# Optimization experiments

Hardware: AMD Instinct MI355X
Metric: run time of the kernel (lower is better)

The kernel has to match this reference:

```python
import jax, jax.numpy as jnp
import numpy as np

EPS = 1e-5  # torch InstanceNorm2d default eps


def _attend(x_q, x_kv, Wq, Wk, Wv, Wo):
    # x_q, x_kv: [B, N, C]
    B, N, _ = x_q.shape
    q = x_q @ Wq            # [B, N, CH]
    k = x_kv @ Wk           # [B, N, CH]
    v = x_kv @ Wv           # [B, N, CH]
    CH = q.shape[-1]
    # rearrange 'b n c -> n (b c)' : [N, B*CH]; the torch repeat across batch
    # is redundant (same K/V for every query sample), so we keep one copy.
    kcat = jnp.transpose(k, (1, 0, 2)).reshape(N, B * CH)
    vcat = jnp.transpose(v, (1, 0, 2)).reshape(N, B * CH)
    # scores[b, i, j] = sum_n q[b, n, i] * kcat[n, j]  -> [B, CH, B*CH]
    scores = jnp.einsum('bni,nj->bij', q, kcat)
    # InstanceNorm2d(1): per-sample normalization over the (CH, B*CH) plane
    mu = scores.mean(axis=(1, 2), keepdims=True)
    var = scores.var(axis=(1, 2), keepdims=True)  # biased var, matches torch
    scores = (scores - mu) * jax.lax.rsqrt(var + EPS)
    attn = jax.nn.softmax(scores, axis=-1)        # softmax over j (dim=3)
    # ctx[b, n, i] = sum_j attn[b, i, j] * vcat[n, j]  -> [B, N, CH]
    ctx = jnp.einsum('bij,nj->bni', attn, vcat)
    return ctx @ Wo  # [B, N, C]


def setup_inputs() -> dict:
    key = jax.random.key(0)
    k0, k1, k2, k3, k4 = jax.random.split(key, 5)
    C, H = 64, 8
    CH = C * H
    emb = jax.random.normal(k0, (16, 2048, C), dtype=jnp.float32)
    s = 0.02
    Wq = jax.random.normal(k1, (C, CH), dtype=jnp.float32) * s
    Wk = jax.random.normal(k2, (C, CH), dtype=jnp.float32) * s
    Wv = jax.random.normal(k3, (C, CH), dtype=jnp.float32) * s
    Wo = jax.random.normal(k4, (CH, C), dtype=jnp.float32) * s
    return {"emb": emb, "Wq": Wq, "Wk": Wk, "Wv": Wv, "Wo": Wo}


def reference(emb, Wq, Wk, Wv, Wo):
    emb_l, emb_u = jnp.split(emb, 2, axis=0)
    emb_u_sg = jax.lax.stop_gradient(emb_u)  # emb_u is detached in the torch code
    out_u2l = _attend(emb_u_sg, emb_l, Wq, Wk, Wv, Wo)
    out_l2u = _attend(emb_l, emb_u_sg, Wq, Wk, Wv, Wo)
    return jnp.concatenate([out_l2u, out_u2l], axis=0)
```

## Files before the change

### kernel.cpp

```cpp
#include <hip/hip_runtime.h>
#include <hip/hip_fp16.h>

#define EPS 1e-5f

typedef __attribute__((ext_vector_type(8))) _Float16 half8;
typedef __attribute__((ext_vector_type(4))) _Float16 half4;
typedef __attribute__((ext_vector_type(4))) float float4v;

__device__ __forceinline__ float rv_from(const float* sums2, int db)
{
    float s1 = 0.f, s2 = 0.f;
#pragma unroll
    for (int p = 0; p < 8; p++) {
        s1 += sums2[(db * 8 + p) * 2];
        s2 += sums2[(db * 8 + p) * 2 + 1];
    }
    const float inv = 1.f / 2097152.f;
    float mu = s1 * inv;
    float var = s2 * inv - mu * mu;
    return rsqrtf(var + EPS);
}

__global__ __launch_bounds__(256)
void convT_k(const float* __restrict__ emb, const float* __restrict__ Wq,
             const float* __restrict__ Wk, const float* __restrict__ Wv,
             const float* __restrict__ Wo, __half* __restrict__ emb16,
             __half* __restrict__ embT16, __half* __restrict__ WkT16,
             __half* __restrict__ Wo16, __half* __restrict__ Wv16,
             float* __restrict__ GWQpart, float* __restrict__ wsp,
             __half* __restrict__ WqT16h, __half* __restrict__ WqT16l)
{
    __shared__ __align__(16) char smem[18432];
    const int tid = threadIdx.x;
    const int bid = blockIdx.x;

    if (bid < 256) {
        __half (*T)[136] = (__half(*)[136])smem;
        const int bb = bid >> 4;
        const int t0 = (bid & 15) * 128;
        const float* src = emb + (long long)bb * 131072 + (long long)t0 * 64;
        __half* d16 = emb16 + (long long)bb * 131072 + (long long)t0 * 64;
#pragma unroll
        for (int it = 0; it < 8; it++) {
            int e = (tid + it * 256) * 4;
            int t = e >> 6, c = e & 63;
            float4 v = *(const float4*)(src + t * 64 + c);
            half4 h;
            h[0] = (_Float16)v.x; h[1] = (_Float16)v.y;
            h[2] = (_Float16)v.z; h[3] = (_Float16)v.w;
            *(half4*)(d16 + t * 64 + c) = h;
            T[c + 0][t] = (__half)h[0];
            T[c + 1][t] = (__half)h[1];
            T[c + 2][t] = (__half)h[2];
            T[c + 3][t] = (__half)h[3];
        }
        __syncthreads();
        __half* dT = embT16 + (long long)bb * 131072 + t0;
#pragma unroll
        for (int it = 0; it < 4; it++) {
            int e = (tid + it * 256) * 8;
            int c = e >> 7, tt = e & 127;
            *(half8*)(dT + (long long)c * 2048 + tt) = *(const half8*)&T[c][tt];
        }
    } else if (bid < 272) {
        float (*t)[65] = (float(*)[65])smem;
        const int which = (bid - 256) >> 3;
        const int c0 = ((bid - 256) & 7) * 64;
        const int c = tid & 63, r4 = tid >> 6;
        if (which == 0) {
#pragma unroll
            for (int rr = r4; rr < 64; rr += 4)
                t[rr][c] = Wk[rr * 512 + c0 + c];
            __syncthreads();
#pragma unroll
            for (int rr = r4; rr < 64; rr += 4)
                WkT16[(c0 + rr) * 64 + c] = __float2half(t[c][rr]);
        } else {
#pragma unroll
            for (int rr = r4; rr < 64; rr += 4)
                t[rr][c] = Wo[(c0 + rr) * 64 + c];
            __syncthreads();
#pragma unroll
            for (int rr = r4; rr < 64; rr += 4)
                Wo16[rr * 512 + c0 + c] = __float2half(t[c][rr]);
        }
    } else if (bid < 280) {
        const int base = (bid - 272) * 4096;
#pragma unroll
        for (int it = 0; it < 4; it++) {
            int e = base + (tid + it * 256) * 4;
            float4 v = *(const float4*)(Wv + e);
            *(__half2*)(Wv16 + e)     = __floats2half2_rn(v.x, v.y);
            *(__half2*)(Wv16 + e + 2) = __floats2half2_rn(v.z, v.w);
        }
    } else if (bid < 296) {
        float (*Wl)[68] = (float(*)[68])smem;
        const int t2 = bid - 280;
        const int which = t2 >> 3;
        const int sl = t2 & 7;
        const int i0 = sl * 64;
        const float* W = which ? Wq : Wk;
        float* Gout = GWQpart + (long long)(which * 8 + sl) * 4096;
#pragma unroll
        for (int it = 0; it < 4; it++) {
            int e = tid + it * 256;
            int cc = e >> 4, i4 = (e & 15) * 4;
            *(float4*)&Wl[cc][i4] = *(const float4*)(W + cc * 512 + i0 + i4);
        }
        __syncthreads();
        if (tid < 64) {
            float s = 0.f;
#pragma unroll
            for (int j = 0; j < 64; j++) s += Wl[tid][j];
            wsp[(which * 8 + sl) * 64 + tid] = s;
        }
        const int cr = tid >> 2, cg = (tid & 3) * 16;
        float p[16] = {};
        for (int k = 0; k < 64; k++) {
            float a = Wl[cr][k];
#pragma unroll
            for (int j = 0; j < 16; j++) p[j] += a * Wl[cg + j][k];
        }
#pragma unroll
        for (int j = 0; j < 16; j++)
            Gout[cr * 64 + cg + j] = p[j];
    } else {
        float (*t)[65] = (float(*)[65])smem;
        const int i0 = (bid - 296) * 64;
        const int c = tid & 63, r4 = tid >> 6;
#pragma unroll
        for (int rr = r4; rr < 64; rr += 4)
            t[rr][c] = Wq[rr * 512 + i0 + c];
        __syncthreads();
#pragma unroll
        for (int rr = r4; rr < 64; rr += 4) {
            float x = t[c][rr];
            __half h = __float2half(x);
            WqT16h[(i0 + rr) * 64 + c] = h;
            WqT16l[(i0 + rr) * 64 + c] = __float2half(x - __half2float(h));
        }
    }
}

__global__ __launch_bounds__(256)
void gram_k(const __half* __restrict__ embT16, float* __restrict__ Gpart)
{
    const int tid = threadIdx.x, bid = blockIdx.x;
    const int ks = bid >> 6, z6 = bid & 63;
    const int b = z6 >> 3, bp = z6 & 7;
    const int lane = tid & 63, w = tid >> 6, q = lane >> 4, l16 = lane & 15;

    const __half* Arow = embT16 + (long long)b * 131072 +
                         (long long)(w * 16 + l16) * 2048 + ks * 256 + q * 8;
    const __half* Bbase = embT16 + 1048576 + (long long)bp * 131072 +
                          (long long)l16 * 2048 + ks * 256 + q * 8;

    float4v acc[4];
#pragma unroll
    for (int nt = 0; nt < 4; nt++) acc[nt] = (float4v)0.f;

#pragma unroll
    for (int t0 = 0; t0 < 256; t0 += 32) {
        half8 af = *(const half8*)(Arow + t0);
        half8 bf[4];
#pragma unroll
        for (int nt = 0; nt < 4; nt++)
            bf[nt] = *(const half8*)(Bbase + nt * 32768 + t0);
#pragma unroll
        for (int nt = 0; nt < 4; nt++)
            acc[nt] = __builtin_amdgcn_mfma_f32_16x16x32_f16(af, bf[nt], acc[nt], 0, 0, 0);
    }

    float* Gz = Gpart + (long long)ks * 262144 + (long long)z6 * 4096;
#pragma unroll
    for (int nt = 0; nt < 4; nt++)
#pragma unroll
        for (int t = 0; t < 4; t++) {
            int m = w * 16 + q * 4 + t;
            Gz[m * 64 + nt * 16 + l16] = acc[nt][t];
        }
}

__global__ __launch_bounds__(256)
void stats2_k(const float* __restrict__ Gpart, const float* __restrict__ GWQpart,
              const float* __restrict__ wsp, __half* __restrict__ GT16h,
              __half* __restrict__ GT16l, float* __restrict__ sums2)
{
    __shared__ float Graw[64][68], Gs[64][68], GQs[64][68], GWs[64][68];
    __shared__ float wqsS[64], wksS[64];
    const int tid = threadIdx.x;
    const int z = blockIdx.x;
    const int d = z >> 6, b = (z >> 3) & 7, bp = z & 7;
    const int zm = d ? (bp * 8 + b) : (b * 8 + bp);

    for (int f = tid * 4; f < 4096; f += 1024) {
        float4 g = make_float4(0.f, 0.f, 0.f, 0.f);
        float4 gw = g, gq = g;
#pragma unroll
        for (int s = 0; s < 8; s++) {
            float4 p = *(const float4*)(Gpart + (long long)s * 262144 + (long long)zm * 4096 + f);
            g.x += p.x; g.y += p.y; g.z += p.z; g.w += p.w;
            float4 w1 = *(const float4*)(GWQpart + (long long)s * 4096 + f);
            gw.x += w1.x; gw.y += w1.y; gw.z += w1.z; gw.w += w1.w;
            float4 q1 = *(const float4*)(GWQpart + (long long)(8 + s) * 4096 + f);
            gq.x += q1.x; gq.y += q1.y; gq.z += q1.z; gq.w += q1.w;
        }
        int rr = f >> 6, cc = f & 63;
        *(float4*)&Graw[rr][cc] = g;
        *(float4*)&GWs[rr][cc] = gw;
        *(float4*)&GQs[rr][cc] = gq;
    }
    if (tid < 64) {
        float a = 0.f, bsum = 0.f;
#pragma unroll
        for (int s = 0; s < 8; s++) {
            bsum += wsp[s * 64 + tid];
            a    += wsp[(8 + s) * 64 + tid];
        }
        wqsS[tid] = a; wksS[tid] = bsum;
    }
    __syncthreads();
    for (int e = tid; e < 4096; e += 256) {
        int rr = e >> 6, cc = e & 63;
        Gs[rr][cc] = d ? Graw[cc][rr] : Graw[rr][cc];
    }
    __syncthreads();
    for (int e = tid; e < 4096; e += 256) {
        int cp = e >> 6, c = e & 63;
        float g = Gs[c][cp];
        __half h = __float2half(g);
        GT16h[(long long)z * 4096 + e] = h;
        GT16l[(long long)z * 4096 + e] = __float2half(g - __half2float(h));
    }

    const int r = tid >> 2;
    const int c0 = (tid & 3) * 16;
    float p1[16] = {}, p2[16] = {};
    for (int k = 0; k < 64; k++) {
        float gq = GQs[r][k], g = Gs[r][k];
#pragma unroll
        for (int j = 0; j < 16; j++) {
            p1[j] += gq * Gs[k][c0 + j];
            p2[j] += g  * GWs[k][c0 + j];
        }
    }
    float s2 = 0.f;
#pragma unroll
    for (int j = 0; j < 16; j++) s2 += p1[j] * p2[j];
    float s1 = 0.f;
    const float wq = wqsS[r];
#pragma unroll
    for (int j = 0; j < 16; j++) s1 += wq * Gs[r][c0 + j] * wksS[c0 + j];

    const int lane = tid & 63, w = tid >> 6;
#pragma unroll
    for (int off = 32; off; off >>= 1) {
        s1 += __shfl_down(s1, off, 64);
        s2 += __shfl_down(s2, off, 64);
    }
    __shared__ float r1[4], r2[4];
    if (lane == 0) { r1[w] = s1; r2[w] = s2; }
    __syncthreads();
    if (tid == 0) {
        sums2[z * 2]     = r1[0] + r1[1] + r1[2] + r1[3];
        sums2[z * 2 + 1] = r2[0] + r2[1] + r2[2] + r2[3];
    }
}

__global__ __launch_bounds__(256)
void mfma_ms(const __half* __restrict__ WqT16h, const __half* __restrict__ WqT16l,
             const __half* __restrict__ GT16h, const __half* __restrict__ GT16l,
             const __half* __restrict__ WkT16, const __half* __restrict__ Wv16,
             const float* __restrict__ sums2, float* __restrict__ rsp,
             __half* __restrict__ Mt)
{
    __shared__ __half Es[128][72];
    __shared__ __half Pt[128][72];

    const int tid = threadIdx.x;
    const int z = blockIdx.x;
    const int it = blockIdx.y;
    const int db = z >> 3, bp = z & 7;
    const int i0base = it * 128;

    const int lane = tid & 63, w = tid >> 6, q = lane >> 4, l16 = lane & 15;
    const float rv = rv_from(sums2, db);

    {
        const __half* Wh = WqT16h + (long long)i0base * 64;
        const __half* Wl = WqT16l + (long long)i0base * 64;
        const __half* Gh = GT16h + (long long)z * 4096;
        const __half* Gl = GT16l + (long long)z * 4096;
        float4v eacc[2][4];
#pragma unroll
        for (int a = 0; a < 2; a++)
#pragma unroll
            for (int b2 = 0; b2 < 4; b2++) eacc[a][b2] = (float4v)0.f;
#pragma unroll
        for (int kc = 0; kc < 64; kc += 32) {
            half8 ah[2], al[2], bh[4], bl[4];
#pragma unroll
            for (int mt = 0; mt < 2; mt++) {
                const int i = w * 32 + mt * 16 + l16;
                ah[mt] = *(const half8*)(Wh + i * 64 + kc + q * 8);
                al[mt] = *(const half8*)(Wl + i * 64 + kc + q * 8);
            }
#pragma unroll
            for (int nt = 0; nt < 4; nt++) {
                const int cp = nt * 16 + l16;
                bh[nt] = *(const half8*)(Gh + cp * 64 + kc + q * 8);
                bl[nt] = *(const half8*)(Gl + cp * 64 + kc + q * 8);
            }
#pragma unroll
            for (int mt = 0; mt < 2; mt++)
#pragma unroll
                for (int nt = 0; nt < 4; nt++) {
                    eacc[mt][nt] = __builtin_amdgcn_mfma_f32_16x16x32_f16(ah[mt], bh[nt], eacc[mt][nt], 0, 0, 0);
                    eacc[mt][nt] = __builtin_amdgcn_mfma_f32_16x16x32_f16(ah[mt], bl[nt], eacc[mt][nt], 0, 0, 0);
                    eacc[mt][nt] = __builtin_amdgcn_mfma_f32_16x16x32_f16(al[mt], bh[nt], eacc[mt][nt], 0, 0, 0);
                }
        }
#pragma unroll
        for (int mt = 0; mt < 2; mt++)
#pragma unroll
            for (int nt = 0; nt < 4; nt++)
#pragma unroll
                for (int t = 0; t < 4; t++)
                    Es[w * 32 + mt * 16 + q * 4 + t][nt * 16 + l16] =
                        __float2half(eacc[mt][nt][t]);
    }

    float4v macc[2][4];
#pragma unroll
    for (int a = 0; a < 2; a++)
#pragma unroll
        for (int b2 = 0; b2 < 4; b2++) macc[a][b2] = (float4v)0.f;
    float rsacc[2] = {0.f, 0.f};

    for (int ch0 = 0; ch0 < 512; ch0 += 64) {
        float4v sacc[4][2];
#pragma unroll
        for (int a = 0; a < 4; a++)
#pragma unroll
            for (int b2 = 0; b2 < 2; b2++) sacc[a][b2] = (float4v)0.f;
#pragma unroll
        for (int kc = 0; kc < 64; kc += 32) {
            half8 af[4], bf[2];
#pragma unroll
            for (int mt = 0; mt < 4; mt++)
                af[mt] = *(const half8*)(WkT16 +
                    (long long)(ch0 + mt * 16 + l16) * 64 + kc + q * 8);
#pragma unroll
            for (int nt = 0; nt < 2; nt++)
                bf[nt] = *(const half8*)&Es[w * 32 + nt * 16 + l16][kc + q * 8];
#pragma unroll
            for (int mt = 0; mt < 4; mt++)
#pragma unroll
                for (int nt = 0; nt < 2; nt++)
                    sacc[mt][nt] = __builtin_amdgcn_mfma_f32_16x16x32_f16(af[mt], bf[nt], sacc[mt][nt], 0, 0, 0);
        }

#pragma unroll
        for (int nt = 0; nt < 2; nt++) {
            const int i = w * 32 + nt * 16 + l16;
#pragma unroll
            for (int mt = 0; mt < 4; mt++) {
                float e0 = __expf(rv * sacc[mt][nt][0]);
                float e1 = __expf(rv * sacc[mt][nt][1]);
                float e2 = __expf(rv * sacc[mt][nt][2]);
                float e3 = __expf(rv * sacc[mt][nt][3]);
                rsacc[nt] += e0 + e1 + e2 + e3;
                const int ch = mt * 16 + q * 4;
                *(__half2*)&Pt[i][ch]     = __floats2half2_rn(e0, e1);
                *(__half2*)&Pt[i][ch + 2] = __floats2half2_rn(e2, e3);
            }
        }

#pragma unroll
        for (int kc = 0; kc < 64; kc += 32) {
            half8 af2[2], bf2[4];
#pragma unroll
            for (int mt2 = 0; mt2 < 2; mt2++)
                af2[mt2] = *(const half8*)&Pt[w * 32 + mt2 * 16 + l16][kc + q * 8];
#pragma unroll
            for (int nt2 = 0; nt2 < 4; nt2++)
                bf2[nt2] = *(const half8*)(Wv16 +
                    (long long)(nt2 * 16 + l16) * 512 + ch0 + kc + q * 8);
#pragma unroll
            for (int mt2 = 0; mt2 < 2; mt2++)
#pragma unroll
                for (int nt2 = 0; nt2 < 4; nt2++)
                    macc[mt2][nt2] = __builtin_amdgcn_mfma_f32_16x16x32_f16(af2[mt2], bf2[nt2], macc[mt2][nt2], 0, 0, 0);
        }
    }

#pragma unroll
    for (int nt = 0; nt < 2; nt++) {
        float p = rsacc[nt];
        p += __shfl_xor(p, 16, 64);
        p += __shfl_xor(p, 32, 64);
        if (q == 0)
            rsp[(long long)(db * 512 + i0base + w * 32 + nt * 16 + l16) * 8 + bp] = p;
    }
    __syncthreads();

    __half (*MtS)[144] = (__half(*)[144])&Pt[0][0];
    const float sc = 1.f / 4096.f;
#pragma unroll
    for (int mt2 = 0; mt2 < 2; mt2++)
#pragma unroll
        for (int nt2 = 0; nt2 < 4; nt2++) {
            const int cp = nt2 * 16 + l16;
            const int il = w * 32 + mt2 * 16 + q * 4;
#pragma unroll
            for (int t = 0; t < 4; t++)
                MtS[cp][il + t] = __float2half(macc[mt2][nt2][t] * sc);
        }
    __syncthreads();
    __half* Mz = Mt + (long long)z * 32768;
    {
        const int row = tid >> 2, seg = (tid & 3) * 32;
#pragma unroll
        for (int j = 0; j < 4; j++)
            *(half8*)(Mz + (long long)row * 512 + i0base + seg + j * 8) =
                *(const half8*)&MtS[row][seg + j * 8];
    }
}

__global__ __launch_bounds__(256)
void mfma_n(const __half* __restrict__ Mt, const __half* __restrict__ Wo16,
            const float* __restrict__ rsp, __half* __restrict__ NT)
{
    __shared__ __half Mts[64][72];
    __shared__ __half Wos[64][72];
    __shared__ float invrS[64];
    const int tid = threadIdx.x;
    const int db = blockIdx.x >> 3, bp = blockIdx.x & 7;
    const __half* Mz = Mt + (long long)(db * 8 + bp) * 32768;
    const int lane = tid & 63, w = tid >> 6, q = lane >> 4, l16 = lane & 15;

    float4v acc[4];
#pragma unroll
    for (int mt = 0; mt < 4; mt++) acc[mt] = (float4v)0.f;

    const int srow = tid >> 2, sc8 = (tid & 3) * 16;

    for (int i0 = 0; i0 < 512; i0 += 64) {
        __syncthreads();
        if (tid < 64) {
            const float* rp = rsp + (long long)(db * 512 + i0 + tid) * 8;
            float4 a = *(const float4*)rp;
            float4 b = *(const float4*)(rp + 4);
            invrS[tid] = 4096.0f / (a.x + a.y + a.z + a.w + b.x + b.y + b.z + b.w);
        }
        __syncthreads();
#pragma unroll
        for (int h = 0; h < 2; h++) {
            half8 v = *(const half8*)(Mz + (long long)srow * 512 + i0 + sc8 + h * 8);
            half8 o;
#pragma unroll
            for (int j = 0; j < 8; j++)
                o[j] = (_Float16)((float)v[j] * invrS[sc8 + h * 8 + j]);
            *(half8*)&Mts[srow][sc8 + h * 8] = o;
            *(half8*)&Wos[srow][sc8 + h * 8] =
                *(const half8*)(Wo16 + (long long)srow * 512 + i0 + sc8 + h * 8);
        }
        __syncthreads();
#pragma unroll
        for (int kc = 0; kc < 64; kc += 32) {
            half8 af[4];
#pragma unroll
            for (int mt = 0; mt < 4; mt++)
                af[mt] = *(const half8*)&Mts[mt * 16 + l16][kc + q * 8];
            half8 bf = *(const half8*)&Wos[w * 16 + l16][kc + q * 8];
#pragma unroll
            for (int mt = 0; mt < 4; mt++)
                acc[mt] = __builtin_amdgcn_mfma_f32_16x16x32_f16(af[mt], bf, acc[mt], 0, 0, 0);
        }
    }

    __half* Nz = NT + (long long)db * 32768;
    const int o = w * 16 + l16;
#pragma unroll
    for (int mt = 0; mt < 4; mt++) {
        const int k = bp * 64 + mt * 16 + q * 4;
        *(__half2*)(Nz + (long long)o * 512 + k)     = __floats2half2_rn(acc[mt][0], acc[mt][1]);
        *(__half2*)(Nz + (long long)o * 512 + k + 2) = __floats2half2_rn(acc[mt][2], acc[mt][3]);
    }
}

__global__ __launch_bounds__(256)
void mfma_out(const __half* __restrict__ emb16, const __half* __restrict__ NT,
              float* __restrict__ out)
{
    const int tid = threadIdx.x;
    const int db = blockIdx.y;
    const int d = db >> 3;
    const int n0 = blockIdx.x * 128;
    const __half* Xb = emb16 + (long long)(1 - d) * 1048576;
    const __half* Bz = NT + (long long)db * 32768;

    const int lane = tid & 63, w = tid >> 6, q = lane >> 4, l16 = lane & 15;

    float4v acc[2][4];
#pragma unroll
    for (int a = 0; a < 2; a++)
#pragma unroll
        for (int b = 0; b < 4; b++) acc[a][b] = (float4v)0.f;

    for (int bp = 0; bp < 8; bp++) {
        const __half* src = Xb + (long long)bp * 131072 + (long long)n0 * 64;
#pragma unroll
        for (int kc = 0; kc < 64; kc += 32) {
            half8 af[2], bf[4];
#pragma unroll
            for (int mt = 0; mt < 2; mt++)
                af[mt] = *(const half8*)(src + (long long)(w * 32 + mt * 16 + l16) * 64 + kc + q * 8);
#pragma unroll
            for (int ot = 0; ot < 4; ot++)
                bf[ot] = *(const half8*)(Bz + (long long)(ot * 16 + l16) * 512 + bp * 64 + kc + q * 8);
#pragma unroll
            for (int mt = 0; mt < 2; mt++)
#pragma unroll
                for (int ot = 0; ot < 4; ot++)
                    acc[mt][ot] = __builtin_amdgcn_mfma_f32_16x16x32_f16(af[mt], bf[ot], acc[mt][ot], 0, 0, 0);
        }
    }

    float* Od = out + (long long)db * 131072;
#pragma unroll
    for (int mt = 0; mt < 2; mt++)
#pragma unroll
        for (int ot = 0; ot < 4; ot++)
#pragma unroll
            for (int t = 0; t < 4; t++) {
                int n = n0 + w * 32 + mt * 16 + q * 4 + t;
                Od[(long long)n * 64 + ot * 16 + l16] = acc[mt][ot][t];
            }
}

extern "C" void kernel_launch(void* const* d_in, const int* in_sizes, int n_in,
                              void* d_out, int out_size, void* d_ws, size_t ws_size,
                              hipStream_t stream)
{
    const float* emb = (const float*)d_in[0];
    const float* Wq  = (const float*)d_in[1];
    const float* Wk  = (const float*)d_in[2];
    const float* Wv  = (const float*)d_in[3];
    const float* Wo  = (const float*)d_in[4];
    float* out = (float*)d_out;
    float* ws  = (float*)d_ws;

    float* Gpart   = ws;
    float* GWQpart = ws + 2097152;
    float* wsp     = ws + 2162688;
    float* sums2   = ws + 2163712;
    __half* GT16h  = (__half*)(ws + 2163968);
    __half* GT16l  = (__half*)(ws + 2426112);
    float* rsp     = ws + 2688256;
    __half* WkT16  = (__half*)(ws + 2753792);
    __half* Wv16   = (__half*)(ws + 2770176);
    __half* Wo16   = (__half*)(ws + 2786560);
    __half* WqT16h = (__half*)(ws + 2802944);
    __half* WqT16l = (__half*)(ws + 2819328);
    __half* Mt     = (__half*)(ws + 2835712);
    __half* NT     = (__half*)(ws + 4932864);
    __half* emb16  = (__half*)(ws + 5195008);
    __half* embT16 = (__half*)(ws + 6243584);

    convT_k<<<304, 256, 0, stream>>>(emb, Wq, Wk, Wv, Wo, emb16, embT16,
                                     WkT16, Wo16, Wv16, GWQpart, wsp,
                                     WqT16h, WqT16l);

    gram_k<<<512, 256, 0, stream>>>(embT16, Gpart);

    stats2_k<<<128, 256, 0, stream>>>(Gpart, GWQpart, wsp, GT16h, GT16l, sums2);

    mfma_ms<<<dim3(128, 4), 256, 0, stream>>>(WqT16h, WqT16l, GT16h, GT16l,
                                              WkT16, Wv16, sums2, rsp, Mt);

    mfma_n<<<128, 256, 0, stream>>>(Mt, Wo16, rsp, NT);

    mfma_out<<<dim3(16, 16), 256, 0, stream>>>(emb16, NT, out);
}
```

Measured before the change: 171.0 us.

## Double-buffer Wk and Wv tiles in LDS with register prefetch in mfma_ms

Each 64-channel chunk of WkT16 and Wv16 is now staged into double-buffered shared memory, with the next chunk prefetched into registers while the current chunk is computed. This replaces redundant per-wave global loads of the weight fragments with one cooperative load per block, and hides global latency. The cost is about 36KB of extra LDS, which may reduce occupancy, and a block-wide barrier on every iteration.

```diff
diff --git a/kernel.cpp b/kernel.cpp
--- a/kernel.cpp
+++ b/kernel.cpp
@@ -275,6 +275,8 @@
              __half* __restrict__ Mt)
 {
     __shared__ __half Es[128][72];
+    __shared__ __half Wks[2][64][72];
+    __shared__ __half Wvs[2][64][72];
     __shared__ __half Pt[128][72];
 
     const int tid = threadIdx.x;
@@ -285,6 +287,12 @@
 
     const int lane = tid & 63, w = tid >> 6, q = lane >> 4, l16 = lane & 15;
     const float rv = rv_from(sums2, db);
+    const int srow = tid >> 2, sc8 = (tid & 3) * 16;
+
+    half8 gk0 = *(const half8*)(WkT16 + (long long)srow * 64 + sc8);
+    half8 gk1 = *(const half8*)(WkT16 + (long long)srow * 64 + sc8 + 8);
+    half8 gv0 = *(const half8*)(Wv16 + (long long)srow * 512 + sc8);
+    half8 gv1 = *(const half8*)(Wv16 + (long long)srow * 512 + sc8 + 8);
 
     {
         const __half* Wh = WqT16h + (long long)i0base * 64;
@@ -329,6 +337,11 @@
                     Es[w * 32 + mt * 16 + q * 4 + t][nt * 16 + l16] =
                         __float2half(eacc[mt][nt][t]);
     }
+    *(half8*)&Wks[0][srow][sc8]     = gk0;
+    *(half8*)&Wks[0][srow][sc8 + 8] = gk1;
+    *(half8*)&Wvs[0][srow][sc8]     = gv0;
+    *(half8*)&Wvs[0][srow][sc8 + 8] = gv1;
+    __syncthreads();
 
     float4v macc[2][4];
 #pragma unroll
@@ -337,7 +350,17 @@
         for (int b2 = 0; b2 < 4; b2++) macc[a][b2] = (float4v)0.f;
     float rsacc[2] = {0.f, 0.f};
 
-    for (int ch0 = 0; ch0 < 512; ch0 += 64) {
+    int cur = 0;
+    for (int c = 0; c < 8; c++) {
+        const int ch0 = c * 64;
+        if (c < 7) {
+            const int chn = ch0 + 64;
+            gk0 = *(const half8*)(WkT16 + (long long)(chn + srow) * 64 + sc8);
+            gk1 = *(const half8*)(WkT16 + (long long)(chn + srow) * 64 + sc8 + 8);
+            gv0 = *(const half8*)(Wv16 + (long long)srow * 512 + chn + sc8);
+            gv1 = *(const half8*)(Wv16 + (long long)srow * 512 + chn + sc8 + 8);
+        }
+
         float4v sacc[4][2];
 #pragma unroll
         for (int a = 0; a < 4; a++)
@@ -348,8 +371,7 @@
             half8 af[4], bf[2];
 #pragma unroll
             for (int mt = 0; mt < 4; mt++)
-                af[mt] = *(const half8*)(WkT16 +
-                    (long long)(ch0 + mt * 16 + l16) * 64 + kc + q * 8);
+                af[mt] = *(const half8*)&Wks[cur][mt * 16 + l16][kc + q * 8];
 #pragma unroll
             for (int nt = 0; nt < 2; nt++)
                 bf[nt] = *(const half8*)&Es[w * 32 + nt * 16 + l16][kc + q * 8];
@@ -384,14 +406,22 @@
                 af2[mt2] = *(const half8*)&Pt[w * 32 + mt2 * 16 + l16][kc + q * 8];
 #pragma unroll
             for (int nt2 = 0; nt2 < 4; nt2++)
-                bf2[nt2] = *(const half8*)(Wv16 +
-                    (long long)(nt2 * 16 + l16) * 512 + ch0 + kc + q * 8);
+                bf2[nt2] = *(const half8*)&Wvs[cur][nt2 * 16 + l16][kc + q * 8];
 #pragma unroll
             for (int mt2 = 0; mt2 < 2; mt2++)
 #pragma unroll
                 for (int nt2 = 0; nt2 < 4; nt2++)
                     macc[mt2][nt2] = __builtin_amdgcn_mfma_f32_16x16x32_f16(af2[mt2], bf2[nt2], macc[mt2][nt2], 0, 0, 0);
         }
+
+        if (c < 7) {
+            *(half8*)&Wks[cur ^ 1][srow][sc8]     = gk0;
+            *(half8*)&Wks[cur ^ 1][srow][sc8 + 8] = gk1;
+            *(half8*)&Wvs[cur ^ 1][srow][sc8]     = gv0;
+            *(half8*)&Wvs[cur ^ 1][srow][sc8 + 8] = gv1;
+        }
+        __syncthreads();
+        cur ^= 1;
     }
 
 #pragma unroll
@@ -402,7 +432,6 @@
         if (q == 0)
             rsp[(long long)(db * 512 + i0base + w * 32 + nt * 16 + l16) * 8 + bp] = p;
     }
-    __syncthreads();
 
     __half (*MtS)[144] = (__half(*)[144])&Pt[0][0];
     const float sc = 1.f / 4096.f;
```

Result: faster. 156.9 us, median of 2 (-8.3%).
